# Optimization experiments

Hardware: AMD Instinct MI355X
Metric: run time of the kernel (lower is better)

The kernel has to match this reference:

```python
import jax, jax.numpy as jnp
import numpy as np

B, F_C, F_F = 2, 32768, 131072
C_IN, C_OUT, W_DIM, COLOR = 128, 64, 512, 3
K2 = 9
PAD0, PAD1 = 192, 384
ACT_GAIN = float(np.sqrt(2.0))  # lrelu def_gain


def _gather(x, nbr, is_pad, pad):
    # x: [N, C]; nbr: [M, k] indices into [N + pad]; is_pad: [M, k] bool
    padded = jnp.concatenate([x, jnp.zeros((pad, x.shape[1]), x.dtype)], 0)
    g = padded[nbr]  # [M, k, C]
    return jnp.where(is_pad[..., None], jnp.zeros((), x.dtype), g)


def _affine(w, aw, ab):
    # StyleGAN FullyConnectedLayer: runtime weight gain 1/sqrt(fan_in), bias_init=1
    return w @ (aw.T * (1.0 / np.sqrt(aw.shape[1]))) + ab


def _modconv(xg, weight, styles, demodulate=True):
    # xg: [N, k, I]; weight: [O, I, 1, k]; styles: [B, I]
    n, k, ci = xg.shape
    w = weight[:, :, 0, :][None, :, :, :] * styles[:, None, :, None]  # [B,O,I,k]
    if demodulate:
        w = w * jax.lax.rsqrt(jnp.sum(w * w, axis=(2, 3), keepdims=True) + 1e-8)
    xb = xg.reshape(styles.shape[0], -1, k, ci)  # [B,F,k,I]
    return jnp.einsum('bfki,boik->bfo', xb, w).reshape(n, -1)


def _smooth_upsample(x, nbr, is_pad, pad, pool_map):
    # upsample coarse->fine via parent map, then masked neighborhood mean
    xf = x[pool_map]  # [N_fine, C]
    g = _gather(xf, nbr, is_pad, pad)  # [N_fine, k, C]
    cnt = jnp.maximum(jnp.sum(~is_pad, axis=1), 1).astype(x.dtype)
    return jnp.sum(g, axis=1) / cnt[:, None]


def _act(x, gain):
    # clamp_gain(lrelu(x), act_gain*gain, 256*gain)
    y = jnp.where(x >= 0, x, 0.2 * x)
    return jnp.clip(y * (ACT_GAIN * gain), -256.0 * gain, 256.0 * gain)


def setup_inputs():
    key = jax.random.key(0)
    ks = jax.random.split(key, 16)
    x = jax.random.normal(ks[0], (B * F_C, C_IN), jnp.float32)
    img = jax.random.normal(ks[1], (B * F_C, COLOR), jnp.float32)
    ws = jax.random.normal(ks[2], (B, 3, W_DIM), jnp.float32)
    fn0 = jax.random.randint(ks[3], (B * F_C, K2), 0, B * F_C + PAD0, jnp.int32)
    fn1 = jax.random.randint(ks[4], (B * F_F, K2), 0, B * F_F + PAD1, jnp.int32)
    fip0 = jax.random.bernoulli(ks[5], 0.05, (B * F_C, K2))
    fip1 = jax.random.bernoulli(ks[6], 0.05, (B * F_F, K2))
    pool_map0 = jax.random.randint(ks[7], (B * F_F,), 0, B * F_C, jnp.int32)
    a0_w = jax.random.normal(ks[8], (C_IN, W_DIM), jnp.float32)
    a0_b = jnp.ones((C_IN,), jnp.float32)
    W0 = jax.random.normal(ks[9], (C_OUT, C_IN, 1, K2), jnp.float32)
    b0 = jnp.zeros((C_OUT,), jnp.float32)
    ns0 = jnp.zeros((1,), jnp.float32)
    nc0 = jax.random.normal(ks[10], (F_F,), jnp.float32)
    a1_w = jax.random.normal(ks[11], (C_OUT, W_DIM), jnp.float32)
    a1_b = jnp.ones((C_OUT,), jnp.float32)
    W1 = jax.random.normal(ks[12], (C_OUT, C_OUT, 1, K2), jnp.float32)
    b1 = jnp.zeros((C_OUT,), jnp.float32)
    ns1 = jnp.zeros((1,), jnp.float32)
    nc1 = jax.random.normal(ks[13], (F_F,), jnp.float32)
    at_w = jax.random.normal(ks[14], (C_OUT, W_DIM), jnp.float32)
    at_b = jnp.ones((C_OUT,), jnp.float32)
    Wt = jax.random.normal(ks[15], (COLOR, C_OUT, 1, 1), jnp.float32)
    bt = jnp.zeros((COLOR,), jnp.float32)
    return {"x": x, "img": img, "ws": ws, "a0_w": a0_w, "a0_b": a0_b, "W0": W0,
            "b0": b0, "ns0": ns0, "nc0": nc0, "a1_w": a1_w, "a1_b": a1_b,
            "W1": W1, "b1": b1, "ns1": ns1, "nc1": nc1, "at_w": at_w,
            "at_b": at_b, "Wt": Wt, "bt": bt, "fn0": fn0, "fip0": fip0,
            "fn1": fn1, "fip1": fip1, "pool_map0": pool_map0,
            "pad0": PAD0, "pad1": PAD1}


def reference(x, img, ws, a0_w, a0_b, W0, b0, ns0, nc0, a1_w, a1_b, W1, b1, ns1,
              nc1, at_w, at_b, Wt, bt, fn0, fip0, fn1, fip1, pool_map0, pad0, pad1):
    b = ws.shape[0]
    w0, w1, w2 = ws[:, 0], ws[:, 1], ws[:, 2]
    # conv0: coarse gather -> mod conv -> smooth upsample to fine -> noise/bias/act
    s0 = _affine(w0, a0_w, a0_b)
    noise0 = jnp.tile(nc0[None, :], (b, 1)).reshape(-1, 1) * ns0  # noise_mode='const'
    h = _modconv(_gather(x, fn0, fip0, pad0), W0, s0)
    h = _smooth_upsample(h, fn1, fip1, pad1, pool_map0)
    h = _act(h + noise0 + b0[None, :], 1.0)
    # conv1: fine level, no resampler
    s1 = _affine(w1, a1_w, a1_b)
    noise1 = jnp.tile(nc1[None, :], (b, 1)).reshape(-1, 1) * ns1
    h = _modconv(_gather(h, fn1, fip1, pad1), W1, s1)
    h = _act(h + noise1 + b1[None, :], 1.0)
    # torgb: kernel_size=1 -> self index only, no demodulation
    st = _affine(w2, at_w, at_b) * (1.0 / np.sqrt(C_OUT))
    y = _modconv(_gather(h, fn1[:, :1], fip1[:, :1], pad1), Wt, st, demodulate=False)
    y = jnp.clip(y + bt[None, :], -256.0, 256.0)
    img = _smooth_upsample(img, fn1, fip1, pad1, pool_map0) + y
    return (h, img)
```

## Files before the change

kernel.cpp:

```cpp
#include <hip/hip_runtime.h>
#include <hip/hip_bf16.h>

constexpr int F_C   = 32768;
constexpr int F_F   = 131072;
constexpr int N0    = 65536;
constexpr int N1    = 262144;
constexpr int C_IN  = 128;
constexpr int W_DIM = 512;
constexpr int K2c   = 9;
constexpr float RS512     = 0.04419417382415922f;
constexpr float ACT_GAINc = 1.4142135623730951f;

constexpr size_t FO_S0  = 0;
constexpr size_t FO_S1  = 256;
constexpr size_t FO_ST  = 384;
constexpr size_t OFF_WM0T = 2048;
constexpr size_t OFF_WM1T = OFF_WM0T + 294912;
constexpr size_t OFF_H0   = 458752;
constexpr size_t OFF_HA   = OFF_H0 + (size_t)8388608;
constexpr size_t OFF_YPRE = OFF_H0;

typedef short s16x8 __attribute__((ext_vector_type(8)));
typedef float f32x4 __attribute__((ext_vector_type(4)));

__device__ __forceinline__ float b2f(unsigned short u) {
    union { unsigned int i; float f; } v; v.i = ((unsigned int)u) << 16; return v.f;
}
__device__ __forceinline__ unsigned short f2b(float f) {
    __hip_bfloat16 h = __float2bfloat16(f);
    return *reinterpret_cast<unsigned short*>(&h);
}
__device__ __forceinline__ float waveRedSum(float v) {
    for (int m = 32; m; m >>= 1) v += __shfl_xor(v, m, 64);
    return v;
}
__device__ __forceinline__ float actf(float v) {
    float y = (v >= 0.f) ? v : 0.2f * v;
    y *= ACT_GAINc;
    return fminf(fmaxf(y, -256.f), 256.f);
}

__global__ __launch_bounds__(64)
void k_styles(const float* __restrict__ wsF,
              const float* __restrict__ a0w, const float* __restrict__ a0b,
              const float* __restrict__ a1w, const float* __restrict__ a1b,
              const float* __restrict__ atw, const float* __restrict__ atb,
              float* __restrict__ fr)
{
    int bid = blockIdx.x, lane = threadIdx.x;
    int bb, ii, ll, row; const float *aw, *ab; float* dst; float post = 1.f;
    if (bid < 256)      { bb = bid >> 7;             ii = bid & 127; ll = 0; aw = a0w; ab = a0b; dst = fr + FO_S0; row = 128; }
    else if (bid < 384) { int t = bid - 256; bb = t >> 6; ii = t & 63; ll = 1; aw = a1w; ab = a1b; dst = fr + FO_S1; row = 64; }
    else                { int t = bid - 384; bb = t >> 6; ii = t & 63; ll = 2; aw = atw; ab = atb; dst = fr + FO_ST; row = 64; post = 0.125f; }
    const float* wsv = wsF + (size_t)(bb * 3 + ll) * W_DIM;
    const float* awr = aw + (size_t)ii * W_DIM;
    float s = 0.f;
    for (int j = lane; j < W_DIM; j += 64) s += wsv[j] * awr[j];
    s = waveRedSum(s);
    if (lane == 0) dst[bb * row + ii] = (s * RS512 + ab[ii]) * post;
}

__global__ __launch_bounds__(256)
void k_wmod(const float* __restrict__ W0,
            const float* __restrict__ W1,
            const float* __restrict__ fr,
            unsigned short* __restrict__ wm0T,
            unsigned short* __restrict__ wm1T)
{
    int bo = blockIdx.x, tid = threadIdx.x;
    int b, o, CI, NE; const float* W; const float* S; unsigned short* dst;
    if (bo < 128) { b = bo >> 6; o = bo & 63; CI = 128; NE = 1152; W = W0; S = fr + FO_S0; dst = wm0T; }
    else { int t = bo - 128; b = t >> 6; o = t & 63; CI = 64; NE = 576; W = W1; S = fr + FO_S1; dst = wm1T; }
    const float* Wo = W + (size_t)o * NE;
    const float* Sb = S + (size_t)b * CI;
    float ss = 0.f;
    for (int idx = tid; idx < NE; idx += 256) {
        int i = idx / K2c;
        float p = Wo[idx] * Sb[i];
        ss += p * p;
    }
    __shared__ float red[4];
    float s = waveRedSum(ss);
    if ((tid & 63) == 0) red[tid >> 6] = s;
    __syncthreads();
    float d = rsqrtf(red[0] + red[1] + red[2] + red[3] + 1e-8f);
    for (int idx = tid; idx < NE; idx += 256) {
        int i = idx / K2c, kk = idx - i * K2c;
        dst[((size_t)(b * K2c + kk) * 64 + o) * CI + i] = f2b(Wo[idx] * Sb[i] * d);
    }
}

__global__ __launch_bounds__(256)
void k_layer0(const float* __restrict__ xF,
              const int*  __restrict__ fn0,
              const int*  __restrict__ fip0,
              const unsigned short* __restrict__ wm0T,
              unsigned short* __restrict__ h0B)
{
    __shared__ unsigned short A_lds[64 * 136];
    __shared__ unsigned short W_lds[64 * 136];
    __shared__ int snbr[64];
    const int tid  = threadIdx.x;
    const int g0   = blockIdx.x * 64;
    const int b    = g0 / F_C;
    const int wave = tid >> 6, lane = tid & 63;
    const int lg   = lane >> 4, lr = lane & 15;
    f32x4 acc[4] = {};
    for (int kk = 0; kk < K2c; ++kk) {
        __syncthreads();
        if (tid < 64) {
            int g   = g0 + tid;
            int nbr = fn0[(size_t)g * K2c + kk];
            int pd  = fip0[(size_t)g * K2c + kk];
            snbr[tid] = (!pd && nbr < N0) ? nbr : -1;
        }
        __syncthreads();
        {
            int node = tid >> 2, seg = tid & 3;
            int nbr  = snbr[node];
            unsigned short tmp[32];
            if (nbr >= 0) {
                const float4* src = (const float4*)(xF + (size_t)nbr * C_IN + seg * 32);
                #pragma unroll
                for (int q = 0; q < 8; ++q) {
                    float4 f = src[q];
                    tmp[q*4+0] = f2b(f.x); tmp[q*4+1] = f2b(f.y);
                    tmp[q*4+2] = f2b(f.z); tmp[q*4+3] = f2b(f.w);
                }
            } else {
                #pragma unroll
                for (int q = 0; q < 32; ++q) tmp[q] = 0;
            }
            uint4* dstA = (uint4*)(A_lds + node * 136 + seg * 32);
            #pragma unroll
            for (int q = 0; q < 4; ++q) dstA[q] = ((const uint4*)tmp)[q];
            const uint4* wsrc = (const uint4*)(wm0T + ((size_t)(b * K2c + kk) * 64 + node) * C_IN + seg * 32);
            uint4* dstW = (uint4*)(W_lds + node * 136 + seg * 32);
            #pragma unroll
            for (int q = 0; q < 4; ++q) dstW[q] = wsrc[q];
        }
        __syncthreads();
        #pragma unroll
        for (int ks = 0; ks < 4; ++ks) {
            int kb = ks * 32 + lg * 8;
            s16x8 af = *(const s16x8*)(A_lds + (wave * 16 + lr) * 136 + kb);
            #pragma unroll
            for (int nt = 0; nt < 4; ++nt) {
                s16x8 bf = *(const s16x8*)(W_lds + (nt * 16 + lr) * 136 + kb);
                acc[nt] = __builtin_amdgcn_mfma_f32_16x16x32_bf16(af, bf, acc[nt], 0, 0, 0);
            }
        }
    }
    #pragma unroll
    for (int nt = 0; nt < 4; ++nt) {
        int o = nt * 16 + lr;
        #pragma unroll
        for (int r = 0; r < 4; ++r) {
            int node = g0 + wave * 16 + lg * 4 + r;
            h0B[(size_t)node * 64 + o] = f2b(acc[nt][r]);
        }
    }
}

__global__ __launch_bounds__(256)
void k_ha(const unsigned short* __restrict__ h0B,
          const int*  __restrict__ fn1,
          const int*  __restrict__ fip1,
          const int*  __restrict__ pool,
          const float* __restrict__ nc0,
          const float* __restrict__ ns0,
          const float* __restrict__ b0,
          unsigned short* __restrict__ haB)
{
    __shared__ int   pmArr[288];
    __shared__ int   vArr[288];
    __shared__ float invCnt[32];
    const int tid = threadIdx.x;
    const int n0  = blockIdx.x * 32;
    for (int idx = tid; idx < 288; idx += 256) {
        int fn = fn1[(size_t)n0 * K2c + idx];
        int ip = fip1[(size_t)n0 * K2c + idx];
        int v  = !ip;
        int pm = -1;
        if (v && fn < N1) pm = pool[fn];
        pmArr[idx] = pm;
        vArr[idx]  = v;
    }
    __syncthreads();
    if (tid < 32) {
        int c = 0;
        #pragma unroll
        for (int k = 0; k < K2c; ++k) c += vArr[tid * K2c + k];
        invCnt[tid] = 1.f / (float)(c > 0 ? c : 1);
    }
    __syncthreads();
    const int wave = tid >> 6, lane = tid & 63;
    const float nsc  = ns0[0];
    const float bias = b0[lane];
    for (int jj = 0; jj < 8; ++jj) {
        int node = wave * 8 + jj;
        int g    = n0 + node;
        float acc = 0.f;
        #pragma unroll
        for (int k = 0; k < K2c; ++k) {
            int pm = pmArr[node * K2c + k];
            int pc = pm >= 0 ? pm : 0;
            float val = b2f(h0B[(size_t)pc * 64 + lane]);
            acc += (pm >= 0) ? val : 0.f;
        }
        float hu = acc * invCnt[node];
        float v  = hu + nc0[g & (F_F - 1)] * nsc + bias;
        haB[(size_t)g * 64 + lane] = f2b(actf(v));
    }
}

__global__ __launch_bounds__(256, 2)
void k_layer1(const unsigned short* __restrict__ haB,
              const int*  __restrict__ fn1,
              const int*  __restrict__ fip1,
              const unsigned short* __restrict__ wm1T,
              const float* __restrict__ nc1,
              const float* __restrict__ ns1,
              const float* __restrict__ b1,
              const float* __restrict__ stS,
              const float* __restrict__ WtF,
              float* __restrict__ hOut,
              float* __restrict__ yPre2)
{
    __shared__ unsigned short W_lds[9 * 64 * 64];
    const int tid  = threadIdx.x;
    const int g0   = blockIdx.x * 256;
    const int b    = g0 / F_F;
    const int wave = tid >> 6, lane = tid & 63;
    const int lg   = lane >> 4, lr = lane & 15;
    const int wbase = g0 + wave * 64;
    const unsigned short* wtap = wm1T + (size_t)b * K2c * 4096;

    #pragma unroll
    for (int t = 0; t < 18; ++t) {
        int idx = tid + 256 * t;
        int tap = idx >> 9;
        int rem = idx & 511;
        int row = rem >> 3, c = rem & 7;
        uint4 v = ((const uint4*)wtap)[idx];
        *(uint4*)(&W_lds[tap * 4096 + row * 64 + ((c ^ (row & 7)) << 3)]) = v;
    }

    int nbrk[4][9];
    #pragma unroll
    for (int rg = 0; rg < 4; ++rg) {
        int row = wbase + rg * 16 + lr;
        #pragma unroll
        for (int k = 0; k < 9; ++k) {
            int fn = fn1[(size_t)row * 9 + k];
            int ip = fip1[(size_t)row * 9 + k];
            nbrk[rg][k] = (!ip && fn < N1) ? fn : -1;
        }
    }
    __syncthreads();

    f32x4 acc[4][4] = {};
    #pragma unroll
    for (int kk = 0; kk < 9; ++kk) {
        s16x8 bf[2][4];
        #pragma unroll
        for (int h = 0; h < 2; ++h)
            #pragma unroll
            for (int nt = 0; nt < 4; ++nt) {
                int row = nt * 16 + lr;
                bf[h][nt] = *(const s16x8*)(&W_lds[kk * 4096 + row * 64 + (((h * 4 + lg) ^ (row & 7)) << 3)]);
            }
        #pragma unroll
        for (int rg = 0; rg < 4; ++rg) {
            int nbr = nbrk[rg][kk];
            int pc  = nbr >= 0 ? nbr : 0;
            const uint4* ap = (const uint4*)(haB + (size_t)pc * 64) + lg;
            uint4 a0 = ap[0], a1 = ap[4];
            if (nbr < 0) { a0 = uint4{0,0,0,0}; a1 = uint4{0,0,0,0}; }
            s16x8 af0 = *reinterpret_cast<const s16x8*>(&a0);
            s16x8 af1 = *reinterpret_cast<const s16x8*>(&a1);
            #pragma unroll
            for (int nt = 0; nt < 4; ++nt)
                acc[rg][nt] = __builtin_amdgcn_mfma_f32_16x16x32_bf16(af0, bf[0][nt], acc[rg][nt], 0, 0, 0);
            #pragma unroll
            for (int nt = 0; nt < 4; ++nt)
                acc[rg][nt] = __builtin_amdgcn_mfma_f32_16x16x32_bf16(af1, bf[1][nt], acc[rg][nt], 0, 0, 0);
        }
    }

    const float nsc = ns1[0];
    #pragma unroll
    for (int rg = 0; rg < 4; ++rg) {
        float p00[4] = {}, p01[4] = {}, p02[4] = {};
        float p10[4] = {}, p11[4] = {}, p12[4] = {};
        #pragma unroll
        for (int nt = 0; nt < 4; ++nt) {
            int o = nt * 16 + lr;
            float bias = b1[o];
            float st0  = stS[o], st1 = stS[64 + o];
            float wt0 = WtF[o], wt1 = WtF[64 + o], wt2 = WtF[128 + o];
            float w00 = wt0 * st0, w01 = wt1 * st0, w02 = wt2 * st0;
            float w10 = wt0 * st1, w11 = wt1 * st1, w12 = wt2 * st1;
            #pragma unroll
            for (int r = 0; r < 4; ++r) {
                int node = wbase + rg * 16 + lg * 4 + r;
                float v  = actf(acc[rg][nt][r] + nc1[node & (F_F - 1)] * nsc + bias);
                hOut[(size_t)node * 64 + o] = v;
                p00[r] += v * w00; p01[r] += v * w01; p02[r] += v * w02;
                p10[r] += v * w10; p11[r] += v * w11; p12[r] += v * w12;
            }
        }
        #pragma unroll
        for (int m = 1; m < 16; m <<= 1) {
            #pragma unroll
            for (int r = 0; r < 4; ++r) {
                p00[r] += __shfl_xor(p00[r], m, 64);
                p01[r] += __shfl_xor(p01[r], m, 64);
                p02[r] += __shfl_xor(p02[r], m, 64);
                p10[r] += __shfl_xor(p10[r], m, 64);
                p11[r] += __shfl_xor(p11[r], m, 64);
                p12[r] += __shfl_xor(p12[r], m, 64);
            }
        }
        if (lr == 0) {
            #pragma unroll
            for (int r = 0; r < 4; ++r) {
                int node = wbase + rg * 16 + lg * 4 + r;
                yPre2[(size_t)node * 6 + 0] = p00[r];
                yPre2[(size_t)node * 6 + 1] = p01[r];
                yPre2[(size_t)node * 6 + 2] = p02[r];
                yPre2[(size_t)node * 6 + 3] = p10[r];
                yPre2[(size_t)node * 6 + 4] = p11[r];
                yPre2[(size_t)node * 6 + 5] = p12[r];
            }
        }
    }
}

__global__ __launch_bounds__(256)
void k_rgb(const float* __restrict__ yPre2,
           const float* __restrict__ imgF,
           const int*  __restrict__ fn1,
           const int*  __restrict__ fip1,
           const int*  __restrict__ pool,
           const float* __restrict__ btF,
           float* __restrict__ outImg)
{
    const int n = blockIdx.x * 256 + threadIdx.x;
    const int bOut = n / F_F;
    int fn[K2c], ip[K2c];
    #pragma unroll
    for (int k = 0; k < K2c; ++k) {
        fn[k] = fn1[(size_t)n * K2c + k];
        ip[k] = fip1[(size_t)n * K2c + k];
    }
    int pm[K2c], cnt = 0;
    #pragma unroll
    for (int k = 0; k < K2c; ++k) {
        int v  = !ip[k];
        cnt   += v;
        pm[k]  = (v && fn[k] < N1) ? pool[fn[k]] : -1;
    }
    float sr = 0.f, sg = 0.f, sb = 0.f;
    #pragma unroll
    for (int k = 0; k < K2c; ++k) {
        int   pc = pm[k] >= 0 ? pm[k] : 0;
        float m  = pm[k] >= 0 ? 1.f : 0.f;
        sr += m * imgF[(size_t)pc * 3 + 0];
        sg += m * imgF[(size_t)pc * 3 + 1];
        sb += m * imgF[(size_t)pc * 3 + 2];
    }
    int nb0 = (!ip[0] && fn[0] < N1) ? fn[0] : -1;
    float y0 = 0.f, y1 = 0.f, y2 = 0.f;
    if (nb0 >= 0) {
        const float* yp = yPre2 + (size_t)nb0 * 6 + bOut * 3;
        y0 = yp[0]; y1 = yp[1]; y2 = yp[2];
    }
    float ic = 1.f / (float)(cnt > 0 ? cnt : 1);
    y0 = fminf(fmaxf(y0 + btF[0], -256.f), 256.f);
    y1 = fminf(fmaxf(y1 + btF[1], -256.f), 256.f);
    y2 = fminf(fmaxf(y2 + btF[2], -256.f), 256.f);
    outImg[(size_t)n * 3 + 0] = sr * ic + y0;
    outImg[(size_t)n * 3 + 1] = sg * ic + y1;
    outImg[(size_t)n * 3 + 2] = sb * ic + y2;
}

extern "C" void kernel_launch(void* const* d_in, const int* in_sizes, int n_in,
                              void* d_out, int out_size, void* d_ws, size_t ws_size,
                              hipStream_t stream)
{
    const float* xF   = (const float*)d_in[0];
    const float* imgF = (const float*)d_in[1];
    const float* wsF  = (const float*)d_in[2];
    const float* a0w  = (const float*)d_in[3];
    const float* a0b  = (const float*)d_in[4];
    const float* W0w  = (const float*)d_in[5];
    const float* b0w  = (const float*)d_in[6];
    const float* ns0  = (const float*)d_in[7];
    const float* nc0  = (const float*)d_in[8];
    const float* a1w  = (const float*)d_in[9];
    const float* a1b  = (const float*)d_in[10];
    const float* W1w  = (const float*)d_in[11];
    const float* b1w  = (const float*)d_in[12];
    const float* ns1  = (const float*)d_in[13];
    const float* nc1  = (const float*)d_in[14];
    const float* atw  = (const float*)d_in[15];
    const float* atb  = (const float*)d_in[16];
    const float* WtF  = (const float*)d_in[17];
    const float* btF  = (const float*)d_in[18];
    const int* fn0  = (const int*)d_in[19];
    const int* fip0 = (const int*)d_in[20];
    const int* fn1  = (const int*)d_in[21];
    const int* fip1 = (const int*)d_in[22];
    const int* pool = (const int*)d_in[23];

    char* wsb = (char*)d_ws;
    float* fr = (float*)wsb;
    unsigned short* wm0T = (unsigned short*)(wsb + OFF_WM0T);
    unsigned short* wm1T = (unsigned short*)(wsb + OFF_WM1T);
    unsigned short* h0B  = (unsigned short*)(wsb + OFF_H0);
    unsigned short* haB  = (unsigned short*)(wsb + OFF_HA);
    float* yPre2         = (float*)(wsb + OFF_YPRE);

    float* hOut   = (float*)d_out;
    float* imgOut = hOut + (size_t)N1 * 64;

    hipLaunchKernelGGL(k_styles, dim3(512), dim3(64), 0, stream,
                       wsF, a0w, a0b, a1w, a1b, atw, atb, fr);
    hipLaunchKernelGGL(k_wmod, dim3(256), dim3(256), 0, stream,
                       W0w, W1w, fr, wm0T, wm1T);
    hipLaunchKernelGGL(k_layer0, dim3(N0 / 64), dim3(256), 0, stream,
                       xF, fn0, fip0, wm0T, h0B);
    hipLaunchKernelGGL(k_ha, dim3(N1 / 32), dim3(256), 0, stream,
                       h0B, fn1, fip1, pool, nc0, ns0, b0w, haB);
    hipLaunchKernelGGL(k_layer1, dim3(N1 / 256), dim3(256), 0, stream,
                       haB, fn1, fip1, wm1T, nc1, ns1, b1w,
                       fr + FO_ST, WtF, hOut, yPre2);
    hipLaunchKernelGGL(k_rgb, dim3(N1 / 256), dim3(256), 0, stream,
                       yPre2, imgF, fn1, fip1, pool, btF, imgOut);
}
```

Baseline: 200.0 us.

## Pre-convert x to bf16 and restructure layer0 as register-gather MFMA over all taps

Adds a kernel that converts the coarse input features to bf16 once, so the per-tap gathers read half the bytes and skip repeated conversions. Layer0 now processes 256 nodes per block. It stages all nine tap weight tiles in swizzled LDS, split across two channel halves, and preloads neighbour indices into registers. Each wave then loads A fragments straight from global memory into the MFMAs, with no per-tap LDS staging or barriers. Layer1 moves to 512-thread blocks so the shared weight tile serves twice as many nodes, at the cost of one extra launch and higher register pressure.

```diff
diff --git a/kernel.cpp b/kernel.cpp
--- a/kernel.cpp
+++ b/kernel.cpp
@@ -19,6 +19,7 @@
 constexpr size_t OFF_H0   = 458752;
 constexpr size_t OFF_HA   = OFF_H0 + (size_t)8388608;
 constexpr size_t OFF_YPRE = OFF_H0;
+constexpr size_t OFF_XB   = OFF_HA;
 
 typedef short s16x8 __attribute__((ext_vector_type(8)));
 typedef float f32x4 __attribute__((ext_vector_type(4)));
@@ -91,75 +92,96 @@
 }
 
 __global__ __launch_bounds__(256)
-void k_layer0(const float* __restrict__ xF,
+void k_xcvt(const float* __restrict__ xF, unsigned short* __restrict__ xB)
+{
+    int i = blockIdx.x * 256 + threadIdx.x;
+    float4 f = ((const float4*)xF)[i];
+    union { unsigned short u[4]; uint2 v; } t;
+    t.u[0] = f2b(f.x); t.u[1] = f2b(f.y); t.u[2] = f2b(f.z); t.u[3] = f2b(f.w);
+    ((uint2*)xB)[i] = t.v;
+}
+
+__global__ __launch_bounds__(256, 4)
+void k_layer0(const unsigned short* __restrict__ xB,
               const int*  __restrict__ fn0,
               const int*  __restrict__ fip0,
               const unsigned short* __restrict__ wm0T,
               unsigned short* __restrict__ h0B)
 {
-    __shared__ unsigned short A_lds[64 * 136];
-    __shared__ unsigned short W_lds[64 * 136];
-    __shared__ int snbr[64];
+    __shared__ unsigned short W_lds[9 * 64 * 64];
     const int tid  = threadIdx.x;
-    const int g0   = blockIdx.x * 64;
+    const int g0   = blockIdx.x * 256;
     const int b    = g0 / F_C;
     const int wave = tid >> 6, lane = tid & 63;
     const int lg   = lane >> 4, lr = lane & 15;
-    f32x4 acc[4] = {};
-    for (int kk = 0; kk < K2c; ++kk) {
+    const int wbase = g0 + wave * 64;
+    const unsigned short* wtap = wm0T + (size_t)b * K2c * 64 * C_IN;
+
+    int nbrk[4][9];
+    #pragma unroll
+    for (int rg = 0; rg < 4; ++rg) {
+        int row = wbase + rg * 16 + lr;
+        #pragma unroll
+        for (int k = 0; k < 9; ++k) {
+            int fn = fn0[(size_t)row * 9 + k];
+            int ip = fip0[(size_t)row * 9 + k];
+            nbrk[rg][k] = (!ip && fn < N0) ? fn : -1;
+        }
+    }
+
+    f32x4 acc[4][4] = {};
+    for (int h = 0; h < 2; ++h) {
         __syncthreads();
-        if (tid < 64) {
-            int g   = g0 + tid;
-            int nbr = fn0[(size_t)g * K2c + kk];
-            int pd  = fip0[(size_t)g * K2c + kk];
-            snbr[tid] = (!pd && nbr < N0) ? nbr : -1;
+        #pragma unroll
+        for (int t = 0; t < 18; ++t) {
+            int idx = tid + 256 * t;
+            int tap = idx >> 9;
+            int rem = idx & 511;
+            int row = rem >> 3, cc = rem & 7;
+            uint4 v = *(const uint4*)(wtap + ((size_t)tap * 64 + row) * C_IN + h * 64 + cc * 8);
+            *(uint4*)(&W_lds[tap * 4096 + row * 64 + ((cc ^ (row & 7)) << 3)]) = v;
         }
         __syncthreads();
-        {
-            int node = tid >> 2, seg = tid & 3;
-            int nbr  = snbr[node];
-            unsigned short tmp[32];
-            if (nbr >= 0) {
-                const float4* src = (const float4*)(xF + (size_t)nbr * C_IN + seg * 32);
+        #pragma unroll
+        for (int kk = 0; kk < 9; ++kk) {
+            s16x8 bf[2][4];
+            #pragma unroll
+            for (int c2 = 0; c2 < 2; ++c2)
                 #pragma unroll
-                for (int q = 0; q < 8; ++q) {
-                    float4 f = src[q];
-                    tmp[q*4+0] = f2b(f.x); tmp[q*4+1] = f2b(f.y);
-                    tmp[q*4+2] = f2b(f.z); tmp[q*4+3] = f2b(f.w);
+                for (int nt = 0; nt < 4; ++nt) {
+                    int row = nt * 16 + lr;
+                    bf[c2][nt] = *(const s16x8*)(&W_lds[kk * 4096 + row * 64 + (((c2 * 4 + lg) ^ (row & 7)) << 3)]);
                 }
-            } else {
+            #pragma unroll
+            for (int rg = 0; rg < 4; ++rg) {
+                int nbr = nbrk[rg][kk];
+                int pc  = nbr >= 0 ? nbr : 0;
+                const uint4* ap = (const uint4*)(xB + (size_t)pc * C_IN) + lg;
+                uint4 a0 = ap[h * 8];
+                uint4 a1 = ap[h * 8 + 4];
+                if (nbr < 0) { a0 = uint4{0,0,0,0}; a1 = uint4{0,0,0,0}; }
+                s16x8 af0 = *reinterpret_cast<const s16x8*>(&a0);
+                s16x8 af1 = *reinterpret_cast<const s16x8*>(&a1);
                 #pragma unroll
-                for (int q = 0; q < 32; ++q) tmp[q] = 0;
-            }
-            uint4* dstA = (uint4*)(A_lds + node * 136 + seg * 32);
-            #pragma unroll
-            for (int q = 0; q < 4; ++q) dstA[q] = ((const uint4*)tmp)[q];
-            const uint4* wsrc = (const uint4*)(wm0T + ((size_t)(b * K2c + kk) * 64 + node) * C_IN + seg * 32);
-            uint4* dstW = (uint4*)(W_lds + node * 136 + seg * 32);
-            #pragma unroll
-            for (int q = 0; q < 4; ++q) dstW[q] = wsrc[q];
-        }
-        __syncthreads();
-        #pragma unroll
-        for (int ks = 0; ks < 4; ++ks) {
-            int kb = ks * 32 + lg * 8;
-            s16x8 af = *(const s16x8*)(A_lds + (wave * 16 + lr) * 136 + kb);
-            #pragma unroll
-            for (int nt = 0; nt < 4; ++nt) {
-                s16x8 bf = *(const s16x8*)(W_lds + (nt * 16 + lr) * 136 + kb);
-                acc[nt] = __builtin_amdgcn_mfma_f32_16x16x32_bf16(af, bf, acc[nt], 0, 0, 0);
-            }
-        }
-    }
-    #pragma unroll
-    for (int nt = 0; nt < 4; ++nt) {
-        int o = nt * 16 + lr;
-        #pragma unroll
-        for (int r = 0; r < 4; ++r) {
-            int node = g0 + wave * 16 + lg * 4 + r;
-            h0B[(size_t)node * 64 + o] = f2b(acc[nt][r]);
-        }
-    }
+                for (int nt = 0; nt < 4; ++nt)
+                    acc[rg][nt] = __builtin_amdgcn_mfma_f32_16x16x32_bf16(af0, bf[0][nt], acc[rg][nt], 0, 0, 0);
+                #pragma unroll
+                for (int nt = 0; nt < 4; ++nt)
+                    acc[rg][nt] = __builtin_amdgcn_mfma_f32_16x16x32_bf16(af1, bf[1][nt], acc[rg][nt], 0, 0, 0);
+            }
+        }
+    }
+    #pragma unroll
+    for (int rg = 0; rg < 4; ++rg)
+        #pragma unroll
+        for (int nt = 0; nt < 4; ++nt) {
+            int o = nt * 16 + lr;
+            #pragma unroll
+            for (int r = 0; r < 4; ++r) {
+                int node = wbase + rg * 16 + lg * 4 + r;
+                h0B[(size_t)node * 64 + o] = f2b(acc[rg][nt][r]);
+            }
+        }
 }
 
 __global__ __launch_bounds__(256)
@@ -214,7 +236,7 @@
     }
 }
 
-__global__ __launch_bounds__(256, 2)
+__global__ __launch_bounds__(512, 4)
 void k_layer1(const unsigned short* __restrict__ haB,
               const int*  __restrict__ fn1,
               const int*  __restrict__ fip1,
@@ -229,7 +251,7 @@
 {
     __shared__ unsigned short W_lds[9 * 64 * 64];
     const int tid  = threadIdx.x;
-    const int g0   = blockIdx.x * 256;
+    const int g0   = blockIdx.x * 512;
     const int b    = g0 / F_F;
     const int wave = tid >> 6, lane = tid & 63;
     const int lg   = lane >> 4, lr = lane & 15;
@@ -237,8 +259,8 @@
     const unsigned short* wtap = wm1T + (size_t)b * K2c * 4096;
 
     #pragma unroll
-    for (int t = 0; t < 18; ++t) {
-        int idx = tid + 256 * t;
+    for (int t = 0; t < 9; ++t) {
+        int idx = tid + 512 * t;
         int tap = idx >> 9;
         int rem = idx & 511;
         int row = rem >> 3, c = rem & 7;
@@ -420,6 +442,7 @@
     unsigned short* wm1T = (unsigned short*)(wsb + OFF_WM1T);
     unsigned short* h0B  = (unsigned short*)(wsb + OFF_H0);
     unsigned short* haB  = (unsigned short*)(wsb + OFF_HA);
+    unsigned short* xB   = (unsigned short*)(wsb + OFF_XB);
     float* yPre2         = (float*)(wsb + OFF_YPRE);
 
     float* hOut   = (float*)d_out;
@@ -429,11 +452,13 @@
                        wsF, a0w, a0b, a1w, a1b, atw, atb, fr);
     hipLaunchKernelGGL(k_wmod, dim3(256), dim3(256), 0, stream,
                        W0w, W1w, fr, wm0T, wm1T);
-    hipLaunchKernelGGL(k_layer0, dim3(N0 / 64), dim3(256), 0, stream,
-                       xF, fn0, fip0, wm0T, h0B);
+    hipLaunchKernelGGL(k_xcvt, dim3((N0 * C_IN) / 4 / 256), dim3(256), 0, stream,
+                       xF, xB);
+    hipLaunchKernelGGL(k_layer0, dim3(N0 / 256), dim3(256), 0, stream,
+                       xB, fn0, fip0, wm0T, h0B);
     hipLaunchKernelGGL(k_ha, dim3(N1 / 32), dim3(256), 0, stream,
                        h0B, fn1, fip1, pool, nc0, ns0, b0w, haB);
-    hipLaunchKernelGGL(k_layer1, dim3(N1 / 256), dim3(256), 0, stream,
+    hipLaunchKernelGGL(k_layer1, dim3(N1 / 512), dim3(512), 0, stream,
                        haB, fn1, fip1, wm1T, nc1, ns1, b1w,
                        fr + FO_ST, WtF, hOut, yPre2);
     hipLaunchKernelGGL(k_rgb, dim3(N1 / 256), dim3(256), 0, stream,
```

Result: slower. 207.3 us (+3.6%).
